# Optimization experiments

Hardware: AMD Instinct MI355X
Metric: run time of the kernel (lower is better)

Reference implementation:

```python
import jax, jax.numpy as jnp
import numpy as np

B, T, F, H, BB = 256, 512, 5, 512, 128  # batch, seq, features, hidden, cfc backbone units


def lecun_tanh(x):
    return 1.7159 * jnp.tanh(0.666 * x)


def setup_inputs() -> dict:
    key = jax.random.key(0)
    ks = jax.random.split(key, 18)
    def p(k, shape, fan_in):
        lim = 1.0 / np.sqrt(fan_in)
        return jax.random.uniform(k, shape, jnp.float32, -lim, lim)
    return {
        "x": jax.random.normal(ks[0], (B, T, F), jnp.float32),
        # ncps LSTMCell: input_map Linear(F,4H,bias=True), recurrent_map Linear(H,4H,bias=False)
        "lstm_Wi": p(ks[1], (4 * H, F), F),
        "lstm_bi": p(ks[2], (4 * H,), F),
        "lstm_Wh": p(ks[3], (4 * H, H), H),
        # CfCCell backbone: Linear(F+H, BB) + lecun_tanh
        "bb_W": p(ks[4], (BB, F + H), F + H),
        "bb_b": p(ks[5], (BB,), F + H),
        # ff1/ff2/time_a/time_b: Linear(BB, H)
        "ff1_W": p(ks[6], (H, BB), BB), "ff1_b": p(ks[7], (H,), BB),
        "ff2_W": p(ks[8], (H, BB), BB), "ff2_b": p(ks[9], (H,), BB),
        "ta_W": p(ks[10], (H, BB), BB), "ta_b": p(ks[11], (H,), BB),
        "tb_W": p(ks[12], (H, BB), BB), "tb_b": p(ks[13], (H,), BB),
        # heads
        "pred_W": p(ks[14], (2, H), H), "pred_b": p(ks[15], (2,), H),
        "en_W": p(ks[16], (1, H), H), "en_b": p(ks[17], (1,), H),
    }


def _forward(x, lstm_Wi, lstm_bi, lstm_Wh, bb_W, bb_b,
             ff1_W, ff1_b, ff2_W, ff2_b, ta_W, ta_b, tb_W, tb_b,
             pred_W, pred_b, en_W, en_b):
    xt = jnp.swapaxes(x, 0, 1)  # [T, B, F]
    h0 = jnp.zeros((x.shape[0], H), x.dtype)
    c0 = jnp.zeros_like(h0)

    def step(carry, x_t):
        h, c = carry
        # mixed-memory LSTM cell (ncps: forget gate has +1.0 bias)
        z = x_t @ lstm_Wi.T + lstm_bi + h @ lstm_Wh.T  # [B, 4H]
        i, ig, fg, og = jnp.split(z, 4, axis=1)
        c_new = c * jax.nn.sigmoid(fg + 1.0) + jnp.tanh(i) * jax.nn.sigmoid(ig)
        h_lstm = jnp.tanh(c_new) * jax.nn.sigmoid(og)
        # CfC cell (mode=default, ts=1.0)
        feat = lecun_tanh(jnp.concatenate([x_t, h_lstm], axis=1) @ bb_W.T + bb_b)  # [B, BB]
        ff1 = jnp.tanh(feat @ ff1_W.T + ff1_b)
        ff2 = jnp.tanh(feat @ ff2_W.T + ff2_b)
        t_interp = jax.nn.sigmoid((feat @ ta_W.T + ta_b) + (feat @ tb_W.T + tb_b))
        h_new = ff1 * (1.0 - t_interp) + t_interp * ff2
        return (h_new, c_new), h_new

    (h_last, c_last), h_seq = jax.lax.scan(step, (h0, c0), xt)
    h_seq = jnp.swapaxes(h_seq, 0, 1)  # [B, T, H]
    y_pred = h_seq @ pred_W.T + pred_b  # [B, T, 2]
    e_pred = h_seq @ en_W.T + en_b      # [B, T, 1]
    return y_pred, e_pred, h_last, c_last


def reference(x, lstm_Wi, lstm_bi, lstm_Wh, bb_W, bb_b,
              ff1_W, ff1_b, ff2_W, ff2_b, ta_W, ta_b, tb_W, tb_b,
              pred_W, pred_b, en_W, en_b):
    return _forward(x, lstm_Wi, lstm_bi, lstm_Wh, bb_W, bb_b,
                    ff1_W, ff1_b, ff2_W, ff2_b, ta_W, ta_b, tb_W, tb_b,
                    pred_W, pred_b, en_W, en_b)
```

## Files before the change

### kernel.cpp

```cpp
#include <hip/hip_runtime.h>

#define Bn   256
#define Tn   512
#define Fn   5
#define Hn   512
#define BBn  128
#define KSn  544
#define KSP  552
#define BBP  136
#define NC   8
#define WPC  32
#define NWG  (NC*WPC)

typedef __attribute__((ext_vector_type(8))) short bf16x8;
typedef __attribute__((ext_vector_type(4))) float f32x4;
typedef unsigned long long u64;

#define WS_BAR   0
#define WS_DC    2048
#define WS_XCC   4096
#define WS_POK   5120
#define WS_PDT   6144
#define WS_H     24576
#define WS_HL    (WS_H   + Bn*KSn*2)
#define WS_FEAT  (WS_HL  + Bn*KSn*2)
#define WS_ARR   WS_FEAT
#define WS_WH    (WS_FEAT + Bn*BBn*2)
#define WS_BB    (WS_WH  + 2048*KSn*2)
#define WS_FF    (WS_BB  + 128*KSn*2)

#define LB_A     0
#define LB_WH    (LB_A + 32*KSP*2)
#define LB_FF    (LB_WH + 64*KSP*2)
#define LB_FT    (LB_FF + 64*BBP*2)
#define DYN_LDS  (LB_FT + 32*BBP*2)

#define YO 0
#define EO (Bn*Tn*2)
#define HO (EO + Bn*Tn)
#define CO (HO + Bn*Hn)

__device__ __forceinline__ unsigned short f2bf(float f) {
  union { float f; unsigned u; } v; v.f = f;
  unsigned r = v.u + 0x7FFFu + ((v.u >> 16) & 1u);
  return (unsigned short)(r >> 16);
}
__device__ __forceinline__ float bf2f(unsigned short u) {
  union { unsigned u; float f; } v; v.u = ((unsigned)u) << 16;
  return v.f;
}
__device__ __forceinline__ float sigm(float x) { return 1.f / (1.f + __expf(-x)); }
__device__ __forceinline__ float tanhx(float x) {
  float e = __expf(2.f * x);
  return 1.f - 2.f / (e + 1.f);
}

__device__ __forceinline__ u64 ldq_agent(const void* p) {
  return __hip_atomic_load((const u64*)p, __ATOMIC_RELAXED, __HIP_MEMORY_SCOPE_AGENT);
}
__device__ __forceinline__ int ldi_agent(const void* p) {
  return __hip_atomic_load((const int*)p, __ATOMIC_RELAXED, __HIP_MEMORY_SCOPE_AGENT);
}
__device__ __forceinline__ void sti_agent(int* p, int v) {
  __hip_atomic_store(p, v, __ATOMIC_RELAXED, __HIP_MEMORY_SCOPE_AGENT);
}

__device__ __forceinline__ void stage32(const char* src, char* dst, int tid) {
  u64 rg[17];
  #pragma unroll
  for (int i = 0; i < 17; ++i) rg[i] = ldq_agent(src + (tid + i * 256) * 8);
  #pragma unroll
  for (int i = 0; i < 17; ++i) {
    int idx = tid + i * 256;
    int r = idx / 136, ch = idx - r * 136;
    *(u64*)(dst + r * (KSP * 2) + ch * 8) = rg[i];
  }
}

__global__ void __launch_bounds__(256) prep_weights(
    const float* __restrict__ Wh, const float* __restrict__ Wi, const float* __restrict__ bbW,
    const float* __restrict__ f1W, const float* __restrict__ f2W,
    const float* __restrict__ taW, const float* __restrict__ tbW, char* __restrict__ ws)
{
  unsigned short* wh = (unsigned short*)(ws + WS_WH);
  unsigned short* bb = (unsigned short*)(ws + WS_BB);
  unsigned short* ff = (unsigned short*)(ws + WS_FF);
  const int n1 = 2048 * KSn, n2 = 128 * KSn, n3 = Hn * BBn;
  const int ntot = n1 + n2 + 4 * n3;
  for (int i = blockIdx.x * blockDim.x + threadIdx.x; i < ntot; i += gridDim.x * blockDim.x) {
    if (i < n1) {
      int c = i / KSn, k = i % KSn;
      float v = (k < 512) ? Wh[c * 512 + k] : ((k < 517) ? Wi[c * 5 + (k - 512)] : 0.f);
      wh[i] = f2bf(v);
    } else if (i < n1 + n2) {
      int j = i - n1; int o = j / KSn, k = j % KSn;
      float v = (k < 512) ? bbW[o * 517 + 5 + k] : ((k < 517) ? bbW[o * 517 + (k - 512)] : 0.f);
      bb[j] = f2bf(v);
    } else {
      int j = i - n1 - n2; int m = j / n3; int r = j % n3;
      const float* src = (m == 0) ? f1W : (m == 1) ? f2W : (m == 2) ? taW : tbW;
      ff[j] = f2bf(src[r]);
    }
  }
}

__device__ __forceinline__ void flag_bar(int* arr, int wg, int e, int tid) {
  __syncthreads();
  if (tid == 0) sti_agent(&arr[wg * 16], e);
  if (tid < 64) {
    int tries = 0;
    for (;;) {
      int v = (tid < 32) ? ldi_agent(&arr[tid * 16]) : e;
      if (__all(v >= e)) break;
      if (++tries >= (1 << 15)) break;
      __builtin_amdgcn_s_sleep(1);
    }
  }
  __syncthreads();
}

__device__ __forceinline__ void slow_bar(int* ctr, int target) {
  __syncthreads();
  if (threadIdx.x == 0) {
    __threadfence();
    atomicAdd(ctr, 1);
    int tries = 0;
    while (__hip_atomic_load(ctr, __ATOMIC_RELAXED, __HIP_MEMORY_SCOPE_AGENT) < target) {
      __builtin_amdgcn_s_sleep(2);
      if (++tries >= (1 << 18)) break;
    }
    __threadfence();
  }
  __syncthreads();
}

__global__ void __launch_bounds__(256, 1) ebl_main(
    const float* __restrict__ x,   const float* __restrict__ bi,
    const float* __restrict__ bbb, const float* __restrict__ f1b, const float* __restrict__ f2b,
    const float* __restrict__ tab, const float* __restrict__ tbb,
    const float* __restrict__ predW, const float* __restrict__ predb,
    const float* __restrict__ enW,   const float* __restrict__ enb,
    float* __restrict__ out, char* __restrict__ ws)
{
  extern __shared__ char lds[];
  __shared__ float lbuf[4][16][36];
  __shared__ int   pflag;

  unsigned short* hsh = (unsigned short*)(ws + WS_H);
  unsigned short* hls = (unsigned short*)(ws + WS_HL);
  const unsigned short* wh  = (const unsigned short*)(ws + WS_WH);
  const unsigned short* bbw = (const unsigned short*)(ws + WS_BB);
  const unsigned short* ffw = (const unsigned short*)(ws + WS_FF);

  const int tid  = threadIdx.x;
  const int lane = tid & 63;
  const int wv   = tid >> 6;
  const int cl   = blockIdx.x & 7;
  const int wg   = blockIdx.x >> 3;
  const int rbase = cl * WPC;
  const int jbase = wg * 16;

  int* cctr = (int*)(ws + WS_BAR) + cl * 32;
  int* dctr = (int*)(ws + WS_DC);
  int* xccb = (int*)(ws + WS_XCC);
  int* pokb = (int*)(ws + WS_POK);
  int* pdat = (int*)(ws + WS_PDT);
  int* arr  = (int*)(ws + WS_ARR) + cl * (32 * 16);

  const int l15 = lane & 15;
  const int l4  = lane >> 4;
  const int cc  = tid & 15;
  const int rr  = tid >> 4;

  for (int idx = tid; idx < 64 * 68; idx += 256) {
    int r = idx / 68, ch = idx - r * 68;
    int g = r >> 4, c = r & 15;
    bf16x8 v = *(const bf16x8*)(wh + (g * 512 + jbase + c) * KSn + ch * 8);
    *(bf16x8*)(lds + LB_WH + r * (KSP * 2) + ch * 16) = v;
  }
  for (int idx = tid; idx < 64 * 16; idx += 256) {
    int r = idx >> 4, ch = idx & 15;
    int m = r >> 4, c = r & 15;
    bf16x8 v = *(const bf16x8*)(ffw + m * (Hn * BBn) + (jbase + c) * BBn + ch * 8);
    *(bf16x8*)(lds + LB_FF + r * (BBP * 2) + ch * 16) = v;
  }

  float hp0[8], hp1[8], hpe[8];
  if (wv == 0) {
    #pragma unroll
    for (int j = 0; j < 8; ++j) {
      hp0[j] = predW[lane * 8 + j];
      hp1[j] = predW[512 + lane * 8 + j];
      hpe[j] = enW[lane * 8 + j];
    }
  }
  float biC[4];
  #pragma unroll
  for (int g = 0; g < 4; ++g) biC[g] = bi[g * 512 + jbase + cc];
  const float fb1 = f1b[jbase + cc], fb2v = f2b[jbase + cc];
  const float fta = tab[jbase + cc], ftb = tbb[jbase + cc];
  float bbBv[2] = { bbb[wv * 32 + l15], bbb[wv * 32 + 16 + l15] };

  float cst0 = 0.f, cst1 = 0.f;

  int xcc;
  asm volatile("s_getreg_b32 %0, hwreg(HW_REG_XCC_ID)" : "=s"(xcc));
  if (tid == 0) { xccb[blockIdx.x] = xcc; pflag = 1; }
  if (tid < Fn) {
    int b = rbase + wg;
    hsh[b * KSn + 512 + tid] = f2bf(x[(b * Tn + 0) * Fn + tid]);
  }
  slow_bar(dctr, NWG);

  int refx = xccb[cl];
  int vx   = xccb[cl + 8 * (tid & 31)];
  const bool fast = (__ballot(vx != refx) == 0ull);

  int ep = 0;
  int slowph = 0;

  if (fast) {
    if (tid == 0) pdat[blockIdx.x * 16] = 1000 + blockIdx.x;
    flag_bar(arr, wg, ++ep, tid);
    { int g = cl + 8 * (tid & 31); if (ldi_agent(&pdat[g * 16]) != 1000 + g) pflag = 0; }
    __syncthreads();
    if (tid == 0) pdat[blockIdx.x * 16] = 777000 + blockIdx.x * 3;
    flag_bar(arr, wg, ++ep, tid);
    { int g = cl + 8 * (tid & 31); if (ldi_agent(&pdat[g * 16]) != 777000 + g * 3) pflag = 0; }
    __syncthreads();
    if (tid == 0) pokb[blockIdx.x] = pflag;
    __syncthreads();
  }
  slow_bar(dctr, 2 * NWG);

  int pv = pokb[cl + 8 * (tid & 31)];
  const bool fastrun = fast && (__ballot(pv == 0) == 0ull);

  const char* hshB = (const char*)hsh + rbase * (KSn * 2);
  const char* hlsB = (const char*)hls + rbase * (KSn * 2);

  for (int t = 0; t < Tn; ++t) {
    if (wv == 0 && t > 0) {
      const int b = rbase + wg;
      u64 q0 = ldq_agent((const char*)hsh + b * (KSn * 2) + lane * 16);
      u64 q1 = ldq_agent((const char*)hsh + b * (KSn * 2) + lane * 16 + 8);
      float s0 = 0.f, s1 = 0.f, se = 0.f;
      #pragma unroll
      for (int j = 0; j < 8; ++j) {
        unsigned short us = (unsigned short)(((j < 4) ? q0 : q1) >> (16 * (j & 3)));
        float hv = bf2f(us);
        s0 += hv * hp0[j]; s1 += hv * hp1[j]; se += hv * hpe[j];
      }
      #pragma unroll
      for (int off = 32; off > 0; off >>= 1) {
        s0 += __shfl_down(s0, off);
        s1 += __shfl_down(s1, off);
        se += __shfl_down(se, off);
      }
      if (lane == 0) {
        out[YO + b * (Tn * 2) + (t - 1) * 2 + 0] = s0 + predb[0];
        out[YO + b * (Tn * 2) + (t - 1) * 2 + 1] = s1 + predb[1];
        out[EO + b * Tn + (t - 1)]               = se + enb[0];
      }
    }
    if (tid < Fn) {
      int b = rbase + wg;
      hls[b * KSn + 512 + tid] = f2bf(x[(b * Tn + t) * Fn + tid]);
    }

    stage32(hshB, lds + LB_A, tid);
    __syncthreads();
    {
      f32x4 acc0 = {0.f, 0.f, 0.f, 0.f}, acc1 = {0.f, 0.f, 0.f, 0.f};
      const char* a0b = lds + LB_A + l15 * (KSP * 2) + l4 * 16;
      const char* a1b = a0b + 16 * (KSP * 2);
      const char* wb  = lds + LB_WH + (wv * 16 + l15) * (KSP * 2) + l4 * 16;
      #pragma unroll
      for (int ks = 0; ks < 17; ++ks) {
        bf16x8 a0 = *(const bf16x8*)(a0b + ks * 64);
        bf16x8 a1 = *(const bf16x8*)(a1b + ks * 64);
        bf16x8 b8 = *(const bf16x8*)(wb + ks * 64);
        acc0 = __builtin_amdgcn_mfma_f32_16x16x32_bf16(a0, b8, acc0, 0, 0, 0);
        acc1 = __builtin_amdgcn_mfma_f32_16x16x32_bf16(a1, b8, acc1, 0, 0, 0);
      }
      *(f32x4*)(&lbuf[wv][l15][l4 * 4])      = acc0;
      *(f32x4*)(&lbuf[wv][l15][16 + l4 * 4]) = acc1;
    }
    __syncthreads();
    {
      float zi0 = lbuf[0][cc][rr]      + biC[0];
      float zg0 = lbuf[1][cc][rr]      + biC[1];
      float zf0 = lbuf[2][cc][rr]      + biC[2];
      float zo0 = lbuf[3][cc][rr]      + biC[3];
      float zi1 = lbuf[0][cc][rr + 16] + biC[0];
      float zg1 = lbuf[1][cc][rr + 16] + biC[1];
      float zf1 = lbuf[2][cc][rr + 16] + biC[2];
      float zo1 = lbuf[3][cc][rr + 16] + biC[3];
      float cn0 = cst0 * sigm(zf0 + 1.f) + tanhx(zi0) * sigm(zg0);
      float cn1 = cst1 * sigm(zf1 + 1.f) + tanhx(zi1) * sigm(zg1);
      float hl0 = tanhx(cn0) * sigm(zo0);
      float hl1 = tanhx(cn1) * sigm(zo1);
      cst0 = cn0; cst1 = cn1;
      const int b0 = rbase + rr, b1 = rbase + rr + 16;
      hls[b0 * KSn + jbase + cc] = f2bf(hl0);
      hls[b1 * KSn + jbase + cc] = f2bf(hl1);
      if (t == Tn - 1) {
        out[CO + b0 * Hn + jbase + cc] = cn0;
        out[CO + b1 * Hn + jbase + cc] = cn1;
      }
    }
    ++ep;
    if (fastrun) flag_bar(arr, wg, ep, tid);
    else { ++slowph; slow_bar(cctr, slowph * WPC); }

    stage32(hlsB, lds + LB_A, tid);
    __syncthreads();
    {
      f32x4 aB00 = {0.f,0.f,0.f,0.f}, aB01 = {0.f,0.f,0.f,0.f};
      f32x4 aB10 = {0.f,0.f,0.f,0.f}, aB11 = {0.f,0.f,0.f,0.f};
      const char* a0b = lds + LB_A + l15 * (KSP * 2) + l4 * 16;
      const char* a1b = a0b + 16 * (KSP * 2);
      const char* b0r = (const char*)bbw + (wv * 32 + l15) * (KSn * 2) + l4 * 16;
      const char* b1r = b0r + 16 * (KSn * 2);
      #pragma unroll
      for (int ks = 0; ks < 17; ++ks) {
        bf16x8 a0 = *(const bf16x8*)(a0b + ks * 64);
        bf16x8 a1 = *(const bf16x8*)(a1b + ks * 64);
        bf16x8 b0 = *(const bf16x8*)(b0r + ks * 64);
        bf16x8 b1 = *(const bf16x8*)(b1r + ks * 64);
        aB00 = __builtin_amdgcn_mfma_f32_16x16x32_bf16(a0, b0, aB00, 0, 0, 0);
        aB01 = __builtin_amdgcn_mfma_f32_16x16x32_bf16(a0, b1, aB01, 0, 0, 0);
        aB10 = __builtin_amdgcn_mfma_f32_16x16x32_bf16(a1, b0, aB10, 0, 0, 0);
        aB11 = __builtin_amdgcn_mfma_f32_16x16x32_bf16(a1, b1, aB11, 0, 0, 0);
      }
      unsigned short* ft = (unsigned short*)(lds + LB_FT);
      #pragma unroll
      for (int j = 0; j < 4; ++j) {
        int r0 = l4 * 4 + j, r1 = 16 + l4 * 4 + j;
        int c0 = wv * 32 + l15, c1 = wv * 32 + 16 + l15;
        ft[r0 * BBP + c0] = f2bf(1.7159f * tanhx(0.666f * (aB00[j] + bbBv[0])));
        ft[r0 * BBP + c1] = f2bf(1.7159f * tanhx(0.666f * (aB01[j] + bbBv[1])));
        ft[r1 * BBP + c0] = f2bf(1.7159f * tanhx(0.666f * (aB10[j] + bbBv[0])));
        ft[r1 * BBP + c1] = f2bf(1.7159f * tanhx(0.666f * (aB11[j] + bbBv[1])));
      }
    }
    __syncthreads();
    {
      f32x4 ac0 = {0.f, 0.f, 0.f, 0.f}, ac1 = {0.f, 0.f, 0.f, 0.f};
      const char* f0 = lds + LB_FT + l15 * (BBP * 2) + l4 * 16;
      const char* f1 = f0 + 16 * (BBP * 2);
      const char* wb = lds + LB_FF + (wv * 16 + l15) * (BBP * 2) + l4 * 16;
      #pragma unroll
      for (int ks = 0; ks < 4; ++ks) {
        bf16x8 a0 = *(const bf16x8*)(f0 + ks * 64);
        bf16x8 a1 = *(const bf16x8*)(f1 + ks * 64);
        bf16x8 b8 = *(const bf16x8*)(wb + ks * 64);
        ac0 = __builtin_amdgcn_mfma_f32_16x16x32_bf16(a0, b8, ac0, 0, 0, 0);
        ac1 = __builtin_amdgcn_mfma_f32_16x16x32_bf16(a1, b8, ac1, 0, 0, 0);
      }
      *(f32x4*)(&lbuf[wv][l15][l4 * 4])      = ac0;
      *(f32x4*)(&lbuf[wv][l15][16 + l4 * 4]) = ac1;
    }
    __syncthreads();
    {
      float p10 = lbuf[0][cc][rr] + fb1,      p20 = lbuf[1][cc][rr] + fb2v;
      float pa0 = lbuf[2][cc][rr] + fta,      pb0 = lbuf[3][cc][rr] + ftb;
      float p11 = lbuf[0][cc][rr + 16] + fb1, p21 = lbuf[1][cc][rr + 16] + fb2v;
      float pa1 = lbuf[2][cc][rr + 16] + fta, pb1 = lbuf[3][cc][rr + 16] + ftb;
      float f10 = tanhx(p10), f20 = tanhx(p20), ti0 = sigm(pa0 + pb0);
      float f11 = tanhx(p11), f21 = tanhx(p21), ti1 = sigm(pa1 + pb1);
      float hn0 = f10 + ti0 * (f20 - f10);
      float hn1 = f11 + ti1 * (f21 - f11);
      const int b0 = rbase + rr, b1 = rbase + rr + 16;
      hsh[b0 * KSn + jbase + cc] = f2bf(hn0);
      hsh[b1 * KSn + jbase + cc] = f2bf(hn1);
      if (t == Tn - 1) {
        out[HO + b0 * Hn + jbase + cc] = hn0;
        out[HO + b1 * Hn + jbase + cc] = hn1;
      }
    }
    if (t + 1 < Tn && tid < Fn) {
      int b = rbase + wg;
      hsh[b * KSn + 512 + tid] = f2bf(x[(b * Tn + t + 1) * Fn + tid]);
    }
    ++ep;
    if (fastrun) flag_bar(arr, wg, ep, tid);
    else { ++slowph; slow_bar(cctr, slowph * WPC); }
  }

  if (wv == 0) {
    const int b = rbase + wg;
    u64 q0 = ldq_agent((const char*)hsh + b * (KSn * 2) + lane * 16);
    u64 q1 = ldq_agent((const char*)hsh + b * (KSn * 2) + lane * 16 + 8);
    float s0 = 0.f, s1 = 0.f, se = 0.f;
    #pragma unroll
    for (int j = 0; j < 8; ++j) {
      unsigned short us = (unsigned short)(((j < 4) ? q0 : q1) >> (16 * (j & 3)));
      float hv = bf2f(us);
      s0 += hv * hp0[j]; s1 += hv * hp1[j]; se += hv * hpe[j];
    }
    #pragma unroll
    for (int off = 32; off > 0; off >>= 1) {
      s0 += __shfl_down(s0, off);
      s1 += __shfl_down(s1, off);
      se += __shfl_down(se, off);
    }
    if (lane == 0) {
      out[YO + b * (Tn * 2) + (Tn - 1) * 2 + 0] = s0 + predb[0];
      out[YO + b * (Tn * 2) + (Tn - 1) * 2 + 1] = s1 + predb[1];
      out[EO + b * Tn + (Tn - 1)]               = se + enb[0];
    }
  }
}

extern "C" void kernel_launch(void* const* d_in, const int* in_sizes, int n_in,
                              void* d_out, int out_size, void* d_ws, size_t ws_size,
                              hipStream_t stream) {
  const float* x   = (const float*)d_in[0];
  const float* Wi  = (const float*)d_in[1];
  const float* bi  = (const float*)d_in[2];
  const float* Wh  = (const float*)d_in[3];
  const float* bbW = (const float*)d_in[4];
  const float* bbb = (const float*)d_in[5];
  const float* f1W = (const float*)d_in[6];
  const float* f1b = (const float*)d_in[7];
  const float* f2W = (const float*)d_in[8];
  const float* f2b = (const float*)d_in[9];
  const float* taW = (const float*)d_in[10];
  const float* tab = (const float*)d_in[11];
  const float* tbW = (const float*)d_in[12];
  const float* tbb = (const float*)d_in[13];
  const float* pW  = (const float*)d_in[14];
  const float* pb  = (const float*)d_in[15];
  const float* eW  = (const float*)d_in[16];
  const float* eb  = (const float*)d_in[17];
  float* out = (float*)d_out;
  char* ws = (char*)d_ws;

  static_assert(DYN_LDS == 132096, "LDS layout");
  (void)hipFuncSetAttribute((const void*)ebl_main,
                            hipFuncAttributeMaxDynamicSharedMemorySize, DYN_LDS);

  hipMemsetAsync(ws, 0, WS_WH, stream);
  prep_weights<<<2048, 256, 0, stream>>>(Wh, Wi, bbW, f1W, f2W, taW, tbW, ws);

  void* args[] = { (void*)&x, (void*)&bi, (void*)&bbb, (void*)&f1b, (void*)&f2b,
                   (void*)&tab, (void*)&tbb, (void*)&pW, (void*)&pb, (void*)&eW,
                   (void*)&eb, (void*)&out, (void*)&ws };
  hipLaunchCooperativeKernel((const void*)ebl_main, dim3(NWG), dim3(256), args,
                             DYN_LDS, stream);
}
```

Baseline: 9.781 ms.

## Double workgroup to 512 threads and split batch rows across wave pairs

Each workgroup now runs 8 waves instead of 4. Each wave pair splits the 32 batch rows into two 16-row halves, so every wave issues half the MFMAs and does elementwise work for one row instead of two. Staging and weight loads are spread over 512 threads. The flag barrier also skips its sleep for the first few polls. The aim is to cut the per-step critical-path latency of the sequential recurrence by adding more parallel waves. The cost is higher register and scheduling pressure and more threads taking part in each barrier.

New measurement: 10.47 ms. 1.07x slower.

```diff
diff --git a/kernel.cpp b/kernel.cpp
--- a/kernel.cpp
+++ b/kernel.cpp
@@ -11,6 +11,7 @@
 #define NC   8
 #define WPC  32
 #define NWG  (NC*WPC)
+#define NT   512
 
 typedef __attribute__((ext_vector_type(8))) short bf16x8;
 typedef __attribute__((ext_vector_type(4))) float f32x4;
@@ -66,14 +67,19 @@
 }
 
 __device__ __forceinline__ void stage32(const char* src, char* dst, int tid) {
-  u64 rg[17];
+  u64 rg[9];
   #pragma unroll
-  for (int i = 0; i < 17; ++i) rg[i] = ldq_agent(src + (tid + i * 256) * 8);
+  for (int i = 0; i < 9; ++i) {
+    int idx = tid + i * NT;
+    if (idx < 4352) rg[i] = ldq_agent(src + idx * 8);
+  }
   #pragma unroll
-  for (int i = 0; i < 17; ++i) {
-    int idx = tid + i * 256;
-    int r = idx / 136, ch = idx - r * 136;
-    *(u64*)(dst + r * (KSP * 2) + ch * 8) = rg[i];
+  for (int i = 0; i < 9; ++i) {
+    int idx = tid + i * NT;
+    if (idx < 4352) {
+      int r = idx / 136, ch = idx - r * 136;
+      *(u64*)(dst + r * (KSP * 2) + ch * 8) = rg[i];
+    }
   }
 }
 
@@ -113,7 +119,7 @@
       int v = (tid < 32) ? ldi_agent(&arr[tid * 16]) : e;
       if (__all(v >= e)) break;
       if (++tries >= (1 << 15)) break;
-      __builtin_amdgcn_s_sleep(1);
+      if (tries > 2) __builtin_amdgcn_s_sleep(1);
     }
   }
   __syncthreads();
@@ -134,7 +140,7 @@
   __syncthreads();
 }
 
-__global__ void __launch_bounds__(256, 1) ebl_main(
+__global__ void __launch_bounds__(NT, 2) ebl_main(
     const float* __restrict__ x,   const float* __restrict__ bi,
     const float* __restrict__ bbb, const float* __restrict__ f1b, const float* __restrict__ f2b,
     const float* __restrict__ tab, const float* __restrict__ tbb,
@@ -155,6 +161,8 @@
   const int tid  = threadIdx.x;
   const int lane = tid & 63;
   const int wv   = tid >> 6;
+  const int g8   = wv >> 1;
+  const int rb   = wv & 1;
   const int cl   = blockIdx.x & 7;
   const int wg   = blockIdx.x >> 3;
   const int rbase = cl * WPC;
@@ -172,13 +180,13 @@
   const int cc  = tid & 15;
   const int rr  = tid >> 4;
 
-  for (int idx = tid; idx < 64 * 68; idx += 256) {
+  for (int idx = tid; idx < 64 * 68; idx += NT) {
     int r = idx / 68, ch = idx - r * 68;
     int g = r >> 4, c = r & 15;
     bf16x8 v = *(const bf16x8*)(wh + (g * 512 + jbase + c) * KSn + ch * 8);
     *(bf16x8*)(lds + LB_WH + r * (KSP * 2) + ch * 16) = v;
   }
-  for (int idx = tid; idx < 64 * 16; idx += 256) {
+  for (int idx = tid; idx < 64 * 16; idx += NT) {
     int r = idx >> 4, ch = idx & 15;
     int m = r >> 4, c = r & 15;
     bf16x8 v = *(const bf16x8*)(ffw + m * (Hn * BBn) + (jbase + c) * BBn + ch * 8);
@@ -199,9 +207,9 @@
   for (int g = 0; g < 4; ++g) biC[g] = bi[g * 512 + jbase + cc];
   const float fb1 = f1b[jbase + cc], fb2v = f2b[jbase + cc];
   const float fta = tab[jbase + cc], ftb = tbb[jbase + cc];
-  float bbBv[2] = { bbb[wv * 32 + l15], bbb[wv * 32 + 16 + l15] };
-
-  float cst0 = 0.f, cst1 = 0.f;
+  float bbBv[2] = { bbb[g8 * 32 + l15], bbb[g8 * 32 + 16 + l15] };
+
+  float cst = 0.f;
 
   int xcc;
   asm volatile("s_getreg_b32 %0, hwreg(HW_REG_XCC_ID)" : "=s"(xcc));
@@ -271,43 +279,29 @@
     stage32(hshB, lds + LB_A, tid);
     __syncthreads();
     {
-      f32x4 acc0 = {0.f, 0.f, 0.f, 0.f}, acc1 = {0.f, 0.f, 0.f, 0.f};
-      const char* a0b = lds + LB_A + l15 * (KSP * 2) + l4 * 16;
-      const char* a1b = a0b + 16 * (KSP * 2);
-      const char* wb  = lds + LB_WH + (wv * 16 + l15) * (KSP * 2) + l4 * 16;
+      f32x4 acc = {0.f, 0.f, 0.f, 0.f};
+      const char* ab = lds + LB_A + (rb * 16 + l15) * (KSP * 2) + l4 * 16;
+      const char* wb = lds + LB_WH + (g8 * 16 + l15) * (KSP * 2) + l4 * 16;
       #pragma unroll
       for (int ks = 0; ks < 17; ++ks) {
-        bf16x8 a0 = *(const bf16x8*)(a0b + ks * 64);
-        bf16x8 a1 = *(const bf16x8*)(a1b + ks * 64);
+        bf16x8 a  = *(const bf16x8*)(ab + ks * 64);
         bf16x8 b8 = *(const bf16x8*)(wb + ks * 64);
-        acc0 = __builtin_amdgcn_mfma_f32_16x16x32_bf16(a0, b8, acc0, 0, 0, 0);
-        acc1 = __builtin_amdgcn_mfma_f32_16x16x32_bf16(a1, b8, acc1, 0, 0, 0);
-      }
-      *(f32x4*)(&lbuf[wv][l15][l4 * 4])      = acc0;
-      *(f32x4*)(&lbuf[wv][l15][16 + l4 * 4]) = acc1;
+        acc = __builtin_amdgcn_mfma_f32_16x16x32_bf16(a, b8, acc, 0, 0, 0);
+      }
+      *(f32x4*)(&lbuf[g8][l15][rb * 16 + l4 * 4]) = acc;
     }
     __syncthreads();
     {
-      float zi0 = lbuf[0][cc][rr]      + biC[0];
-      float zg0 = lbuf[1][cc][rr]      + biC[1];
-      float zf0 = lbuf[2][cc][rr]      + biC[2];
-      float zo0 = lbuf[3][cc][rr]      + biC[3];
-      float zi1 = lbuf[0][cc][rr + 16] + biC[0];
-      float zg1 = lbuf[1][cc][rr + 16] + biC[1];
-      float zf1 = lbuf[2][cc][rr + 16] + biC[2];
-      float zo1 = lbuf[3][cc][rr + 16] + biC[3];
-      float cn0 = cst0 * sigm(zf0 + 1.f) + tanhx(zi0) * sigm(zg0);
-      float cn1 = cst1 * sigm(zf1 + 1.f) + tanhx(zi1) * sigm(zg1);
-      float hl0 = tanhx(cn0) * sigm(zo0);
-      float hl1 = tanhx(cn1) * sigm(zo1);
-      cst0 = cn0; cst1 = cn1;
-      const int b0 = rbase + rr, b1 = rbase + rr + 16;
-      hls[b0 * KSn + jbase + cc] = f2bf(hl0);
-      hls[b1 * KSn + jbase + cc] = f2bf(hl1);
-      if (t == Tn - 1) {
-        out[CO + b0 * Hn + jbase + cc] = cn0;
-        out[CO + b1 * Hn + jbase + cc] = cn1;
-      }
+      float zi = lbuf[0][cc][rr] + biC[0];
+      float zg = lbuf[1][cc][rr] + biC[1];
+      float zf = lbuf[2][cc][rr] + biC[2];
+      float zo = lbuf[3][cc][rr] + biC[3];
+      float cn = cst * sigm(zf + 1.f) + tanhx(zi) * sigm(zg);
+      float hl = tanhx(cn) * sigm(zo);
+      cst = cn;
+      const int b0 = rbase + rr;
+      hls[b0 * KSn + jbase + cc] = f2bf(hl);
+      if (t == Tn - 1) out[CO + b0 * Hn + jbase + cc] = cn;
     }
     ++ep;
     if (fastrun) flag_bar(arr, wg, ep, tid);
@@ -316,68 +310,51 @@
     stage32(hlsB, lds + LB_A, tid);
     __syncthreads();
     {
-      f32x4 aB00 = {0.f,0.f,0.f,0.f}, aB01 = {0.f,0.f,0.f,0.f};
-      f32x4 aB10 = {0.f,0.f,0.f,0.f}, aB11 = {0.f,0.f,0.f,0.f};
-      const char* a0b = lds + LB_A + l15 * (KSP * 2) + l4 * 16;
-      const char* a1b = a0b + 16 * (KSP * 2);
-      const char* b0r = (const char*)bbw + (wv * 32 + l15) * (KSn * 2) + l4 * 16;
+      f32x4 aB0 = {0.f,0.f,0.f,0.f}, aB1 = {0.f,0.f,0.f,0.f};
+      const char* ab  = lds + LB_A + (rb * 16 + l15) * (KSP * 2) + l4 * 16;
+      const char* b0r = (const char*)bbw + (g8 * 32 + l15) * (KSn * 2) + l4 * 16;
       const char* b1r = b0r + 16 * (KSn * 2);
       #pragma unroll
       for (int ks = 0; ks < 17; ++ks) {
-        bf16x8 a0 = *(const bf16x8*)(a0b + ks * 64);
-        bf16x8 a1 = *(const bf16x8*)(a1b + ks * 64);
+        bf16x8 a  = *(const bf16x8*)(ab + ks * 64);
         bf16x8 b0 = *(const bf16x8*)(b0r + ks * 64);
         bf16x8 b1 = *(const bf16x8*)(b1r + ks * 64);
-        aB00 = __builtin_amdgcn_mfma_f32_16x16x32_bf16(a0, b0, aB00, 0, 0, 0);
-        aB01 = __builtin_amdgcn_mfma_f32_16x16x32_bf16(a0, b1, aB01, 0, 0, 0);
-        aB10 = __builtin_amdgcn_mfma_f32_16x16x32_bf16(a1, b0, aB10, 0, 0, 0);
-        aB11 = __builtin_amdgcn_mfma_f32_16x16x32_bf16(a1, b1, aB11, 0, 0, 0);
+        aB0 = __builtin_amdgcn_mfma_f32_16x16x32_bf16(a, b0, aB0, 0, 0, 0);
+        aB1 = __builtin_amdgcn_mfma_f32_16x16x32_bf16(a, b1, aB1, 0, 0, 0);
       }
       unsigned short* ft = (unsigned short*)(lds + LB_FT);
       #pragma unroll
       for (int j = 0; j < 4; ++j) {
-        int r0 = l4 * 4 + j, r1 = 16 + l4 * 4 + j;
-        int c0 = wv * 32 + l15, c1 = wv * 32 + 16 + l15;
-        ft[r0 * BBP + c0] = f2bf(1.7159f * tanhx(0.666f * (aB00[j] + bbBv[0])));
-        ft[r0 * BBP + c1] = f2bf(1.7159f * tanhx(0.666f * (aB01[j] + bbBv[1])));
-        ft[r1 * BBP + c0] = f2bf(1.7159f * tanhx(0.666f * (aB10[j] + bbBv[0])));
-        ft[r1 * BBP + c1] = f2bf(1.7159f * tanhx(0.666f * (aB11[j] + bbBv[1])));
+        int r0 = rb * 16 + l4 * 4 + j;
+        int c0 = g8 * 32 + l15, c1 = g8 * 32 + 16 + l15;
+        ft[r0 * BBP + c0] = f2bf(1.7159f * tanhx(0.666f * (aB0[j] + bbBv[0])));
+        ft[r0 * BBP + c1] = f2bf(1.7159f * tanhx(0.666f * (aB1[j] + bbBv[1])));
       }
     }
     __syncthreads();
     {
-      f32x4 ac0 = {0.f, 0.f, 0.f, 0.f}, ac1 = {0.f, 0.f, 0.f, 0.f};
-      const char* f0 = lds + LB_FT + l15 * (BBP * 2) + l4 * 16;
-      const char* f1 = f0 + 16 * (BBP * 2);
-      const char* wb = lds + LB_FF + (wv * 16 + l15) * (BBP * 2) + l4 * 16;
+      f32x4 ac = {0.f, 0.f, 0.f, 0.f};
+      const char* fb = lds + LB_FT + (rb * 16 + l15) * (BBP * 2) + l4 * 16;
+      const char* wb = lds + LB_FF + (g8 * 16 + l15) * (BBP * 2) + l4 * 16;
       #pragma unroll
       for (int ks = 0; ks < 4; ++ks) {
-        bf16x8 a0 = *(const bf16x8*)(f0 + ks * 64);
-        bf16x8 a1 = *(const bf16x8*)(f1 + ks * 64);
+        bf16x8 a  = *(const bf16x8*)(fb + ks * 64);
         bf16x8 b8 = *(const bf16x8*)(wb + ks * 64);
-        ac0 = __builtin_amdgcn_mfma_f32_16x16x32_bf16(a0, b8, ac0, 0, 0, 0);
-        ac1 = __builtin_amdgcn_mfma_f32_16x16x32_bf16(a1, b8, ac1, 0, 0, 0);
-      }
-      *(f32x4*)(&lbuf[wv][l15][l4 * 4])      = ac0;
-      *(f32x4*)(&lbuf[wv][l15][16 + l4 * 4]) = ac1;
+        ac = __builtin_amdgcn_mfma_f32_16x16x32_bf16(a, b8, ac, 0, 0, 0);
+      }
+      *(f32x4*)(&lbuf[g8][l15][rb * 16 + l4 * 4]) = ac;
     }
     __syncthreads();
     {
-      float p10 = lbuf[0][cc][rr] + fb1,      p20 = lbuf[1][cc][rr] + fb2v;
-      float pa0 = lbuf[2][cc][rr] + fta,      pb0 = lbuf[3][cc][rr] + ftb;
-      float p11 = lbuf[0][cc][rr + 16] + fb1, p21 = lbuf[1][cc][rr + 16] + fb2v;
-      float pa1 = lbuf[2][cc][rr + 16] + fta, pb1 = lbuf[3][cc][rr + 16] + ftb;
-      float f10 = tanhx(p10), f20 = tanhx(p20), ti0 = sigm(pa0 + pb0);
-      float f11 = tanhx(p11), f21 = tanhx(p21), ti1 = sigm(pa1 + pb1);
-      float hn0 = f10 + ti0 * (f20 - f10);
-      float hn1 = f11 + ti1 * (f21 - f11);
-      const int b0 = rbase + rr, b1 = rbase + rr + 16;
-      hsh[b0 * KSn + jbase + cc] = f2bf(hn0);
-      hsh[b1 * KSn + jbase + cc] = f2bf(hn1);
-      if (t == Tn - 1) {
-        out[HO + b0 * Hn + jbase + cc] = hn0;
-        out[HO + b1 * Hn + jbase + cc] = hn1;
-      }
+      float p1 = lbuf[0][cc][rr] + fb1;
+      float p2 = lbuf[1][cc][rr] + fb2v;
+      float pa = lbuf[2][cc][rr] + fta;
+      float pb = lbuf[3][cc][rr] + ftb;
+      float f1 = tanhx(p1), f2 = tanhx(p2), ti = sigm(pa + pb);
+      float hn = f1 + ti * (f2 - f1);
+      const int b0 = rbase + rr;
+      hsh[b0 * KSn + jbase + cc] = f2bf(hn);
+      if (t == Tn - 1) out[HO + b0 * Hn + jbase + cc] = hn;
     }
     if (t + 1 < Tn && tid < Fn) {
       int b = rbase + wg;
@@ -447,6 +424,6 @@
   void* args[] = { (void*)&x, (void*)&bi, (void*)&bbb, (void*)&f1b, (void*)&f2b,
                    (void*)&tab, (void*)&tbb, (void*)&pW, (void*)&pb, (void*)&eW,
                    (void*)&eb, (void*)&out, (void*)&ws };
-  hipLaunchCooperativeKernel((const void*)ebl_main, dim3(NWG), dim3(256), args,
+  hipLaunchCooperativeKernel((const void*)ebl_main, dim3(NWG), dim3(NT), args,
                              DYN_LDS, stream);
 }
```
